# Performance work log

Measured on AMD Instinct MI355X. Metric: run time of the kernel, lower is better.

The kernel has to match this reference:

```python
import jax, jax.numpy as jnp
import numpy as np

RNN = 64      # rnn_hidden_dim
HID = 64      # hidden_dim
ENC = 3       # encoder_dim
NAG = 8       # n_agents
NACT = 14     # n_actions
CLIP = 0.2    # args.exp_clip (variance floor)
BN_EPS = 1e-5


def _bn(x, g, b):
    # BatchNorm1d in training mode: batch stats, biased variance
    m = x.mean(0)
    v = jnp.mean((x - m) ** 2, 0)
    return g * (x - m) * jax.lax.rsqrt(v + BN_EPS) + b


def setup_inputs() -> dict:
    key = jax.random.key(0)
    ks = jax.random.split(key, 16)
    B, INP = 8192, 96

    def w(k, shape, fan):
        return (jax.random.normal(k, shape, jnp.float32) / np.float32(np.sqrt(fan)))

    d = {}
    d["inputs"] = jax.random.normal(ks[0], (B * NAG, INP), jnp.float32)
    d["hidden_state"] = jax.random.normal(ks[1], (B * NAG, RNN), jnp.float32)
    d["noise"] = jax.random.normal(ks[2], (B, NAG, NAG * ENC), jnp.float32)
    d["fc1_w"] = w(ks[3], (INP, RNN), INP); d["fc1_b"] = jnp.zeros((RNN,), jnp.float32)
    d["w_ih"] = w(ks[4], (RNN, 3 * RNN), RNN); d["w_hh"] = w(ks[5], (RNN, 3 * RNN), RNN)
    d["b_ih"] = jnp.zeros((3 * RNN,), jnp.float32); d["b_hh"] = jnp.zeros((3 * RNN,), jnp.float32)
    d["aw1_w"] = w(ks[6], (RNN, HID), RNN); d["aw1_b"] = jnp.zeros((HID,), jnp.float32)
    d["aw_g"] = jnp.ones((HID,), jnp.float32); d["aw_be"] = jnp.zeros((HID,), jnp.float32)
    d["aw2_w"] = w(ks[7], (HID, 2 * NAG * ENC), HID); d["aw2_b"] = jnp.zeros((2 * NAG * ENC,), jnp.float32)
    d["po1_w"] = w(ks[8], (2 * RNN, HID), 2 * RNN); d["po1_b"] = jnp.zeros((HID,), jnp.float32)
    d["po_g"] = jnp.ones((HID,), jnp.float32); d["po_be"] = jnp.zeros((HID,), jnp.float32)
    d["po2_w"] = w(ks[9], (HID, 2 * ENC), HID); d["po2_b"] = jnp.zeros((2 * ENC,), jnp.float32)
    d["fc2_w"] = w(ks[10], (RNN + ENC * NAG, NACT), RNN + ENC * NAG); d["fc2_b"] = jnp.zeros((NACT,), jnp.float32)
    return d


def reference(inputs, hidden_state, noise,
              fc1_w, fc1_b, w_ih, w_hh, b_ih, b_hh,
              aw1_w, aw1_b, aw_g, aw_be, aw2_w, aw2_b,
              po1_w, po1_b, po_g, po_be, po2_w, po2_b,
              fc2_w, fc2_b):
    B, n, enc = noise.shape[0], NAG, ENC

    x = jax.nn.relu(inputs @ fc1_w + fc1_b)                      # [B*n, RNN]
    h_in = hidden_state.reshape(-1, RNN)

    # torch GRUCell
    gi = x @ w_ih + b_ih
    gh = h_in @ w_hh + b_hh
    ir, iz, i_n = jnp.split(gi, 3, axis=-1)
    hr, hz, h_n = jnp.split(gh, 3, axis=-1)
    r = jax.nn.sigmoid(ir + hr)
    z = jax.nn.sigmoid(iz + hz)
    nt = jnp.tanh(i_n + r * h_n)
    h = (1.0 - z) * nt + z * h_in                                # [B*n, RNN]

    # awareness encoder
    a = jax.nn.relu(_bn(h @ aw1_w + aw1_b, aw_g, aw_be))
    aw = (a @ aw2_w + aw2_b).reshape(B, n, 2 * n * enc)
    mu = aw[:, :, : n * enc]
    sigma = jnp.maximum(jnp.exp(aw[:, :, n * enc:]), CLIP)       # variance
    c = (mu + jnp.sqrt(sigma) * noise).reshape(-1, n * enc)      # rsample

    x_out = jnp.concatenate([h, c], axis=-1) @ fc2_w + fc2_b     # [B*n, NACT]

    # poster branch (training mode): all-pairs concat H[b, j, id] = [h[b,id], h[b,j]]
    hd = jax.lax.stop_gradient(h).reshape(B, n, RNN)
    Hi = jnp.broadcast_to(hd[:, None, :, :], (B, n, n, RNN))     # axis2 = id
    Hj = jnp.broadcast_to(hd[:, :, None, :], (B, n, n, RNN))     # axis1 = j
    H = jnp.concatenate([Hi, Hj], axis=-1).reshape(-1, 2 * RNN)  # [B*n*n, 2*RNN]

    p = jax.nn.relu(_bn(H @ po1_w + po1_b, po_g, po_be))
    out = (p @ po2_w + po2_b).reshape(B, n, 2 * n * enc)
    mu1 = out[:, :, : n * enc]
    sigma1 = jnp.maximum(jnp.exp(out[:, :, n * enc:]), CLIP)

    # KL between diagonal Gaussians (sigma, sigma1 are variances)
    kl = 0.5 * (jnp.log(sigma1 / sigma) + (sigma + (mu - mu1) ** 2) / sigma1 - 1.0)
    KL = kl.mean(axis=-1).mean(axis=-1, keepdims=True)           # [B, 1]
    return (x_out, h, KL)
```

## Files before the change

### kernel.cpp

```cpp
#include <hip/hip_runtime.h>
#include <math.h>

#define NROWS 65536
#define NB    8192
#define STAT_OFF  0
#define P2T_OFF   448
#define WPACK_OFF 832
#define OUT_XOUT 0
#define OUT_H    917504
#define OUT_KL   5111808

typedef __attribute__((ext_vector_type(8))) short bhalf8;
typedef __attribute__((ext_vector_type(4))) float floatx4;
typedef __attribute__((ext_vector_type(4))) unsigned short u16x4;

__device__ __forceinline__ float sigmf(float x) { return 1.0f / (1.0f + __expf(-x)); }
__device__ __forceinline__ float tanhfast(float x) {
    x = fminf(fmaxf(x, -15.f), 15.f);
    float e = __expf(-2.f * x);
    return (1.f - e) / (1.f + e);
}
__device__ __forceinline__ unsigned short f2bf(float f) {
    unsigned int u = __float_as_uint(f);
    u += 0x7FFFu + ((u >> 16) & 1u);
    return (unsigned short)(u >> 16);
}
__device__ __forceinline__ float bf2f(unsigned short s) {
    return __uint_as_float(((unsigned int)s) << 16);
}
__device__ __forceinline__ bhalf8 pack8(float4 a, float4 b) {
    bhalf8 r;
    r[0] = (short)f2bf(a.x); r[1] = (short)f2bf(a.y);
    r[2] = (short)f2bf(a.z); r[3] = (short)f2bf(a.w);
    r[4] = (short)f2bf(b.x); r[5] = (short)f2bf(b.y);
    r[6] = (short)f2bf(b.z); r[7] = (short)f2bf(b.w);
    return r;
}

__global__ void k_prep(const float* __restrict__ fc1_w,
                       const float* __restrict__ w_ih, const float* __restrict__ w_hh,
                       const float* __restrict__ aw1_w, const float* __restrict__ po1_w,
                       const float* __restrict__ aw2_w, const float* __restrict__ fc2_w,
                       const float* __restrict__ po2_w,
                       float* __restrict__ ws)
{
    const int t = threadIdx.x;
    if (blockIdx.x == 0) {
        for (int i = t; i < 448; i += 256) ws[STAT_OFF + i] = 0.f;
        for (int i = t; i < 384; i += 256) {
            int d = i >> 6, c = i & 63;
            ws[P2T_OFF + i] = po2_w[c * 6 + d];
        }
    }

    unsigned short* wpk = (unsigned short*)(ws + WPACK_OFF);
    for (int f = blockIdx.x * 256 + t; f < 5952; f += gridDim.x * 256) {
        int lane, c, tile;
        const float* src;
        int colbase, krowstride, kofs = 0, kmax = 1 << 30, colmax = 16;
        if (f < 768) {
            tile = f / 192; c = (f % 192) / 64; lane = f % 64;
            src = fc1_w; krowstride = 64; colbase = tile * 16;
        } else if (f < 3840) {
            int f2 = f - 768;
            tile = f2 / 128; c = (f2 % 128) / 64; lane = f2 % 64;
            if (tile < 12) { src = w_ih; colbase = tile * 16; }
            else           { src = w_hh; colbase = (tile - 12) * 16; }
            krowstride = 192;
        } else if (f < 5376) {
            int f3 = f - 3840;
            tile = f3 / 128; c = (f3 % 128) / 64; lane = f3 % 64;
            if (tile < 4)       { src = aw1_w; colbase = tile * 16; }
            else if (tile < 8)  { src = po1_w; colbase = (tile - 4) * 16; }
            else                { src = po1_w; colbase = (tile - 8) * 16; kofs = 64; }
            krowstride = 64;
        } else if (f < 5760) {
            int f4 = f - 5376;
            tile = f4 / 128; c = (f4 % 128) / 64; lane = f4 % 64;
            src = aw2_w; krowstride = 48; colbase = tile * 16;
        } else {
            int f5 = f - 5760;
            c = f5 / 64; lane = f5 % 64;
            src = fc2_w; krowstride = 14; colbase = 0;
            kmax = 88; colmax = 14;
        }
        int n = lane & 15, quad = lane >> 4;
        int col = colbase + n;
        unsigned short o[8];
        #pragma unroll
        for (int j = 0; j < 8; j++) {
            int k = c * 32 + quad * 8 + j + kofs;
            float v = (k < kmax && n < colmax) ? src[(size_t)k * krowstride + col] : 0.f;
            o[j] = f2bf(v);
        }
        u16x4 lo, hi;
        lo.x = o[0]; lo.y = o[1]; lo.z = o[2]; lo.w = o[3];
        hi.x = o[4]; hi.y = o[5]; hi.z = o[6]; hi.w = o[7];
        *(u16x4*)&wpk[f * 8]     = lo;
        *(u16x4*)&wpk[f * 8 + 4] = hi;
    }
}

__global__ __launch_bounds__(256, 4) void k_front(
    const float* __restrict__ inp, const float* __restrict__ hin,
    const float* __restrict__ fc1_b,
    const float* __restrict__ b_ih, const float* __restrict__ b_hh,
    const float* __restrict__ aw1_b,
    float* __restrict__ h_out, float* __restrict__ ws)
{
    __shared__ __align__(16) unsigned short s_xb[64 * 80];
    __shared__ float s_stat[448];

    const int t = threadIdx.x;
    const int row0 = blockIdx.x * 64;
    const int lane = t & 63;
    const int w = t >> 6;
    const int n16 = lane & 15;
    const int quad = lane >> 4;
    const int mrow = w * 16 + n16;

    for (int i = t; i < 448; i += 256) s_stat[i] = 0.f;
    __syncthreads();

    const bhalf8* wp1 = (const bhalf8*)((const unsigned short*)(ws + WPACK_OFF));
    const bhalf8* wp2 = wp1 + 768;
    const bhalf8* wp3 = wp1 + 3840;

    bhalf8 ai[3], ahf[2];
    {
        const float* gi = inp + (size_t)(row0 + mrow) * 96 + quad * 8;
        #pragma unroll
        for (int kc = 0; kc < 3; kc++)
            ai[kc] = pack8(*(const float4*)&gi[kc * 32], *(const float4*)&gi[kc * 32 + 4]);
        const float* gh = hin + (size_t)(row0 + mrow) * 64 + quad * 8;
        #pragma unroll
        for (int kc = 0; kc < 2; kc++)
            ahf[kc] = pack8(*(const float4*)&gh[kc * 32], *(const float4*)&gh[kc * 32 + 4]);
    }

    #pragma unroll
    for (int g = 0; g < 4; g++) {
        int col = g * 16 + n16;
        floatx4 d = {0.f, 0.f, 0.f, 0.f};
        d = __builtin_amdgcn_mfma_f32_16x16x32_bf16(ai[0], wp1[(g * 3 + 0) * 64 + lane], d, 0, 0, 0);
        d = __builtin_amdgcn_mfma_f32_16x16x32_bf16(ai[1], wp1[(g * 3 + 1) * 64 + lane], d, 0, 0, 0);
        d = __builtin_amdgcn_mfma_f32_16x16x32_bf16(ai[2], wp1[(g * 3 + 2) * 64 + lane], d, 0, 0, 0);
        float bb = fc1_b[col];
        #pragma unroll
        for (int q = 0; q < 4; q++)
            s_xb[(w * 16 + quad * 4 + q) * 80 + col] = f2bf(fmaxf(d[q] + bb, 0.f));
    }
    bhalf8 ax[2];
    ax[0] = *(const bhalf8*)&s_xb[mrow * 80 + 0  + quad * 8];
    ax[1] = *(const bhalf8*)&s_xb[mrow * 80 + 32 + quad * 8];

    #pragma unroll
    for (int g = 0; g < 4; g++) {
        int col = g * 16 + n16;
        floatx4 dr = {0.f, 0.f, 0.f, 0.f}, dz = {0.f, 0.f, 0.f, 0.f};
        floatx4 dn = {0.f, 0.f, 0.f, 0.f}, dh = {0.f, 0.f, 0.f, 0.f};
        dr = __builtin_amdgcn_mfma_f32_16x16x32_bf16(ax[0],  wp2[((0 + g) * 2 + 0) * 64 + lane], dr, 0, 0, 0);
        dr = __builtin_amdgcn_mfma_f32_16x16x32_bf16(ax[1],  wp2[((0 + g) * 2 + 1) * 64 + lane], dr, 0, 0, 0);
        dr = __builtin_amdgcn_mfma_f32_16x16x32_bf16(ahf[0], wp2[((12 + g) * 2 + 0) * 64 + lane], dr, 0, 0, 0);
        dr = __builtin_amdgcn_mfma_f32_16x16x32_bf16(ahf[1], wp2[((12 + g) * 2 + 1) * 64 + lane], dr, 0, 0, 0);
        dz = __builtin_amdgcn_mfma_f32_16x16x32_bf16(ax[0],  wp2[((4 + g) * 2 + 0) * 64 + lane], dz, 0, 0, 0);
        dz = __builtin_amdgcn_mfma_f32_16x16x32_bf16(ax[1],  wp2[((4 + g) * 2 + 1) * 64 + lane], dz, 0, 0, 0);
        dz = __builtin_amdgcn_mfma_f32_16x16x32_bf16(ahf[0], wp2[((16 + g) * 2 + 0) * 64 + lane], dz, 0, 0, 0);
        dz = __builtin_amdgcn_mfma_f32_16x16x32_bf16(ahf[1], wp2[((16 + g) * 2 + 1) * 64 + lane], dz, 0, 0, 0);
        dn = __builtin_amdgcn_mfma_f32_16x16x32_bf16(ax[0],  wp2[((8 + g) * 2 + 0) * 64 + lane], dn, 0, 0, 0);
        dn = __builtin_amdgcn_mfma_f32_16x16x32_bf16(ax[1],  wp2[((8 + g) * 2 + 1) * 64 + lane], dn, 0, 0, 0);
        dh = __builtin_amdgcn_mfma_f32_16x16x32_bf16(ahf[0], wp2[((20 + g) * 2 + 0) * 64 + lane], dh, 0, 0, 0);
        dh = __builtin_amdgcn_mfma_f32_16x16x32_bf16(ahf[1], wp2[((20 + g) * 2 + 1) * 64 + lane], dh, 0, 0, 0);
        float br_ = b_ih[col] + b_hh[col];
        float bz_ = b_ih[64 + col] + b_hh[64 + col];
        float bin_ = b_ih[128 + col];
        float bhn_ = b_hh[128 + col];
        #pragma unroll
        for (int q = 0; q < 4; q++) {
            int lrow = w * 16 + quad * 4 + q;
            size_t grow = (size_t)(row0 + lrow);
            float r  = sigmf(dr[q] + br_);
            float z  = sigmf(dz[q] + bz_);
            float nt = tanhfast(dn[q] + bin_ + r * (dh[q] + bhn_));
            float hp = hin[grow * 64 + col];
            float h  = (1.f - z) * nt + z * hp;
            h_out[grow * 64 + col] = h;
            s_xb[lrow * 80 + col] = f2bf(h);
        }
    }

    bhalf8 hh0 = *(const bhalf8*)&s_xb[mrow * 80 + 0  + quad * 8];
    bhalf8 hh1 = *(const bhalf8*)&s_xb[mrow * 80 + 32 + quad * 8];

    #pragma unroll
    for (int g = 0; g < 4; g++) {
        int col = g * 16 + n16;
        floatx4 da = {0.f, 0.f, 0.f, 0.f}, du = {0.f, 0.f, 0.f, 0.f}, dv = {0.f, 0.f, 0.f, 0.f};
        da = __builtin_amdgcn_mfma_f32_16x16x32_bf16(hh0, wp3[(g * 2 + 0) * 64 + lane], da, 0, 0, 0);
        da = __builtin_amdgcn_mfma_f32_16x16x32_bf16(hh1, wp3[(g * 2 + 1) * 64 + lane], da, 0, 0, 0);
        du = __builtin_amdgcn_mfma_f32_16x16x32_bf16(hh0, wp3[((4 + g) * 2 + 0) * 64 + lane], du, 0, 0, 0);
        du = __builtin_amdgcn_mfma_f32_16x16x32_bf16(hh1, wp3[((4 + g) * 2 + 1) * 64 + lane], du, 0, 0, 0);
        dv = __builtin_amdgcn_mfma_f32_16x16x32_bf16(hh0, wp3[((8 + g) * 2 + 0) * 64 + lane], dv, 0, 0, 0);
        dv = __builtin_amdgcn_mfma_f32_16x16x32_bf16(hh1, wp3[((8 + g) * 2 + 1) * 64 + lane], dv, 0, 0, 0);
        float ab = aw1_b[col];
        float s1 = 0.f, s2 = 0.f, su = 0.f, suq = 0.f, sv = 0.f, svq = 0.f;
        #pragma unroll
        for (int q = 0; q < 4; q++) {
            float a = da[q] + ab; s1 += a; s2 += a * a;
            float uv = du[q]; su += uv; suq += uv * uv;
            float vv = dv[q]; sv += vv; svq += vv * vv;
        }
        float u8 = su + __shfl_xor(su, 16, 64);
        float v8 = sv + __shfl_xor(sv, 16, 64);
        if ((quad & 1) == 0)
            atomicAdd(&s_stat[384 + col], u8 * v8 * (1.f / 64.f));
        float t1 = s1 + __shfl_xor(s1, 16, 64);   t1 += __shfl_xor(t1, 32, 64);
        float t2 = s2 + __shfl_xor(s2, 16, 64);   t2 += __shfl_xor(t2, 32, 64);
        float t3 = u8 + __shfl_xor(u8, 32, 64);
        float t4 = suq + __shfl_xor(suq, 16, 64); t4 += __shfl_xor(t4, 32, 64);
        float t5 = v8 + __shfl_xor(v8, 32, 64);
        float t6 = svq + __shfl_xor(svq, 16, 64); t6 += __shfl_xor(t6, 32, 64);
        if (quad == 0) {
            atomicAdd(&s_stat[col], t1);
            atomicAdd(&s_stat[64 + col], t2);
            atomicAdd(&s_stat[128 + col], t3);
            atomicAdd(&s_stat[192 + col], t4);
            atomicAdd(&s_stat[256 + col], t5);
            atomicAdd(&s_stat[320 + col], t6);
        }
    }
    __syncthreads();
    if (t < 64) {
        float* gs = ws + STAT_OFF;
        #pragma unroll
        for (int q = 0; q < 7; q++)
            atomicAdd(&gs[q * 64 + t], s_stat[q * 64 + t]);
    }
}

__global__ __launch_bounds__(256) void k_heads(
    const float* __restrict__ h_glob, const float* __restrict__ noise,
    const float* __restrict__ aw1_b, const float* __restrict__ aw2_b,
    const float* __restrict__ fc2_b, const float* __restrict__ po2_b,
    const float* __restrict__ aw_g, const float* __restrict__ aw_be,
    const float* __restrict__ po_g, const float* __restrict__ po_be,
    const float* __restrict__ po1_b,
    const float* __restrict__ ws, float* __restrict__ out)
{
    __shared__ __align__(16) unsigned short s_hb[32 * 104];
    __shared__ __align__(16) unsigned short s_Ub[32 * 80];
    __shared__ __align__(16) unsigned short s_Vb[32 * 80];
    __shared__ float s_ms[32 * 48];
    __shared__ __align__(16) float s_buf[32 * 48];
    __shared__ float s_dv[256];
    __shared__ float s_kl[32];

    const int t = threadIdx.x;
    const int row0 = blockIdx.x * 32;
    const int b0 = blockIdx.x * 4;
    const int lane = t & 63;
    const int w = t >> 6;
    const int n16 = lane & 15;
    const int quad = lane >> 4;
    const int mrow = w * 16 + n16;

    if (t < 64) {
        const float* st = ws + STAT_OFF;
        const float invN = 1.f / 65536.f;
        float am = st[t] * invN;
        float av = st[64 + t] * invN - am * am;
        float asc = aw_g[t] * rsqrtf(av + 1e-5f);
        s_dv[t] = asc;
        s_dv[64 + t] = aw_be[t] - asc * am;
        float Eu = st[128 + t] * invN;
        float vu = st[192 + t] * invN - Eu * Eu;
        float Ev = st[256 + t] * invN;
        float vv = st[320 + t] * invN - Ev * Ev;
        float cov = st[384 + t] * (1.f / 8192.f) - Eu * Ev;
        float my = Eu + Ev + po1_b[t];
        float vy = vu + vv + 2.f * cov;
        float psc = po_g[t] * rsqrtf(vy + 1e-5f);
        s_dv[128 + t] = psc;
        s_dv[192 + t] = po_be[t] + psc * (po1_b[t] - my);
    }

    {
        const float* gh = h_glob + (size_t)row0 * 64;
        for (int i = t; i < 512; i += 256) {
            int r = i >> 4, c4 = (i & 15) * 4;
            float4 v = *(const float4*)&gh[r * 64 + c4];
            u16x4 p; p.x = f2bf(v.x); p.y = f2bf(v.y); p.z = f2bf(v.z); p.w = f2bf(v.w);
            *(u16x4*)&s_hb[r * 104 + c4] = p;
        }
        if (t < 64) {
            int r = t >> 1, c4 = 88 + (t & 1) * 4;
            u16x4 z; z.x = 0; z.y = 0; z.z = 0; z.w = 0;
            *(u16x4*)&s_hb[r * 104 + c4] = z;
        }
    }
    __syncthreads();

    const bhalf8* wp3  = ((const bhalf8*)((const unsigned short*)(ws + WPACK_OFF))) + 3840;
    const bhalf8* wpa2 = wp3 + 1536;
    const bhalf8* wpf2 = wpa2 + 384;
    unsigned short* s_ab = (unsigned short*)s_buf;

    if (w < 2) {
        bhalf8 ah0 = *(const bhalf8*)&s_hb[mrow * 104 + 0  + quad * 8];
        bhalf8 ah1 = *(const bhalf8*)&s_hb[mrow * 104 + 32 + quad * 8];
        #pragma unroll
        for (int g = 0; g < 4; g++) {
            int col = g * 16 + n16;
            floatx4 da = {0.f, 0.f, 0.f, 0.f}, duu = {0.f, 0.f, 0.f, 0.f}, dvv = {0.f, 0.f, 0.f, 0.f};
            da  = __builtin_amdgcn_mfma_f32_16x16x32_bf16(ah0, wp3[(g * 2 + 0) * 64 + lane], da, 0, 0, 0);
            da  = __builtin_amdgcn_mfma_f32_16x16x32_bf16(ah1, wp3[(g * 2 + 1) * 64 + lane], da, 0, 0, 0);
            duu = __builtin_amdgcn_mfma_f32_16x16x32_bf16(ah0, wp3[((4 + g) * 2 + 0) * 64 + lane], duu, 0, 0, 0);
            duu = __builtin_amdgcn_mfma_f32_16x16x32_bf16(ah1, wp3[((4 + g) * 2 + 1) * 64 + lane], duu, 0, 0, 0);
            dvv = __builtin_amdgcn_mfma_f32_16x16x32_bf16(ah0, wp3[((8 + g) * 2 + 0) * 64 + lane], dvv, 0, 0, 0);
            dvv = __builtin_amdgcn_mfma_f32_16x16x32_bf16(ah1, wp3[((8 + g) * 2 + 1) * 64 + lane], dvv, 0, 0, 0);
            float ab = aw1_b[col];
            float asc = s_dv[col], ash = s_dv[64 + col];
            float psc = s_dv[128 + col], psh = s_dv[192 + col];
            #pragma unroll
            for (int q = 0; q < 4; q++) {
                int lrow = w * 16 + quad * 4 + q;
                s_ab[lrow * 80 + col] = f2bf(fmaxf(asc * (da[q] + ab) + ash, 0.f));
                s_Ub[lrow * 80 + col] = f2bf(psc * duu[q]);
                s_Vb[lrow * 80 + col] = f2bf(psc * dvv[q] + psh);
            }
        }
        bhalf8 aa0 = *(const bhalf8*)&s_ab[mrow * 80 + 0  + quad * 8];
        bhalf8 aa1 = *(const bhalf8*)&s_ab[mrow * 80 + 32 + quad * 8];
        #pragma unroll
        for (int g = 0; g < 3; g++) {
            floatx4 d = {0.f, 0.f, 0.f, 0.f};
            d = __builtin_amdgcn_mfma_f32_16x16x32_bf16(aa0, wpa2[(g * 2 + 0) * 64 + lane], d, 0, 0, 0);
            d = __builtin_amdgcn_mfma_f32_16x16x32_bf16(aa1, wpa2[(g * 2 + 1) * 64 + lane], d, 0, 0, 0);
            int col = g * 16 + n16;
            float bb = aw2_b[col];
            #pragma unroll
            for (int q = 0; q < 4; q++) {
                int lrow = w * 16 + quad * 4 + q;
                float v = d[q] + bb;
                s_ms[lrow * 48 + col] = (col < 24) ? v : fmaxf(__expf(v), 0.2f);
            }
        }
    }
    __syncthreads();

    for (int i = t; i < 768; i += 256) {
        int r = i / 24, m = i - r * 24;
        float c = s_ms[r * 48 + m] + sqrtf(s_ms[r * 48 + 24 + m]) * noise[(size_t)(row0 + r) * 24 + m];
        s_hb[r * 104 + 64 + m] = f2bf(c);
    }
    __syncthreads();

    if (w < 2) {
        bhalf8 hc0 = *(const bhalf8*)&s_hb[mrow * 104 + 0  + quad * 8];
        bhalf8 hc1 = *(const bhalf8*)&s_hb[mrow * 104 + 32 + quad * 8];
        bhalf8 hc2 = *(const bhalf8*)&s_hb[mrow * 104 + 64 + quad * 8];
        floatx4 d = {0.f, 0.f, 0.f, 0.f};
        d = __builtin_amdgcn_mfma_f32_16x16x32_bf16(hc0, wpf2[0 * 64 + lane], d, 0, 0, 0);
        d = __builtin_amdgcn_mfma_f32_16x16x32_bf16(hc1, wpf2[1 * 64 + lane], d, 0, 0, 0);
        d = __builtin_amdgcn_mfma_f32_16x16x32_bf16(hc2, wpf2[2 * 64 + lane], d, 0, 0, 0);
        if (n16 < 14) {
            float bb = fc2_b[n16];
            float* xout = out + OUT_XOUT;
            #pragma unroll
            for (int q = 0; q < 4; q++) {
                size_t grow = (size_t)(row0 + w * 16 + quad * 4 + q);
                xout[grow * 14 + n16] = d[q] + bb;
            }
        }
    }
    __syncthreads();

    float* s_out = s_buf;
    {
        const float* p2t = ws + P2T_OFF;
        const int bl = t >> 6;
        const int rem = t & 63;
        const int i_ = rem >> 3;
        const int j_ = rem & 7;
        float acc[6] = {0.f, 0.f, 0.f, 0.f, 0.f, 0.f};
        #pragma unroll
        for (int c = 0; c < 64; c += 8) {
            bhalf8 vb = *(const bhalf8*)&s_Vb[(bl * 8 + i_) * 80 + c];
            bhalf8 ub = *(const bhalf8*)&s_Ub[(bl * 8 + j_) * 80 + c];
            float p[8];
            #pragma unroll
            for (int q = 0; q < 8; q++)
                p[q] = fmaxf(bf2f((unsigned short)ub[q]) + bf2f((unsigned short)vb[q]), 0.f);
            #pragma unroll
            for (int d = 0; d < 6; d++) {
                const float* wd = &p2t[d * 64 + c];
                float s = 0.f;
                #pragma unroll
                for (int q = 0; q < 8; q++) s += p[q] * wd[q];
                acc[d] += s;
            }
        }
        #pragma unroll
        for (int d = 0; d < 6; d++)
            s_out[(bl * 8 + i_) * 48 + j_ * 6 + d] = acc[d] + po2_b[d];
    }
    __syncthreads();

    if (t < 32) {
        float s = 0.f;
        #pragma unroll 4
        for (int m = 0; m < 24; m++) {
            float mu0 = s_ms[t * 48 + m];
            float sg0 = s_ms[t * 48 + 24 + m];
            float mu1 = s_out[t * 48 + m];
            float sg1 = fmaxf(__expf(s_out[t * 48 + 24 + m]), 0.2f);
            float d0 = mu0 - mu1;
            s += __logf(sg1 / sg0) + (sg0 + d0 * d0) / sg1 - 1.f;
        }
        s_kl[t] = s;
    }
    __syncthreads();
    if (t < 4) {
        float s = 0.f;
        #pragma unroll
        for (int i = 0; i < 8; i++) s += s_kl[t * 8 + i];
        out[OUT_KL + b0 + t] = s * (0.5f / 192.f);
    }
}

extern "C" void kernel_launch(void* const* d_in, const int* in_sizes, int n_in,
                              void* d_out, int out_size, void* d_ws, size_t ws_size,
                              hipStream_t stream)
{
    (void)in_sizes; (void)n_in; (void)out_size; (void)ws_size;
    const float* inp   = (const float*)d_in[0];
    const float* hin   = (const float*)d_in[1];
    const float* noise = (const float*)d_in[2];
    const float* fc1_w = (const float*)d_in[3];
    const float* fc1_b = (const float*)d_in[4];
    const float* w_ih  = (const float*)d_in[5];
    const float* w_hh  = (const float*)d_in[6];
    const float* b_ih  = (const float*)d_in[7];
    const float* b_hh  = (const float*)d_in[8];
    const float* aw1_w = (const float*)d_in[9];
    const float* aw1_b = (const float*)d_in[10];
    const float* aw_g  = (const float*)d_in[11];
    const float* aw_be = (const float*)d_in[12];
    const float* aw2_w = (const float*)d_in[13];
    const float* aw2_b = (const float*)d_in[14];
    const float* po1_w = (const float*)d_in[15];
    const float* po1_b = (const float*)d_in[16];
    const float* po_g  = (const float*)d_in[17];
    const float* po_be = (const float*)d_in[18];
    const float* po2_w = (const float*)d_in[19];
    const float* po2_b = (const float*)d_in[20];
    const float* fc2_w = (const float*)d_in[21];
    const float* fc2_b = (const float*)d_in[22];
    float* out = (float*)d_out;
    float* ws  = (float*)d_ws;

    hipLaunchKernelGGL(k_prep,  dim3(24),   dim3(256), 0, stream,
                       fc1_w, w_ih, w_hh, aw1_w, po1_w, aw2_w, fc2_w, po2_w, ws);
    hipLaunchKernelGGL(k_front, dim3(1024), dim3(256), 0, stream,
                       inp, hin, fc1_b, b_ih, b_hh, aw1_b, out + OUT_H, ws);
    hipLaunchKernelGGL(k_heads, dim3(2048), dim3(256), 0, stream,
                       out + OUT_H, noise, aw1_b, aw2_b, fc2_b, po2_b,
                       aw_g, aw_be, po_g, po_be, po1_b, ws, out);
}
```

Measured before the change: 198.6 us.

## Register-block k_front over four row tiles per wave and split k_heads aw1 work

k_front now has each wave process 64 rows (four 16-row tiles), loading each packed weight fragment once and reusing it across four MFMA tiles. Blocks shrink to 128 threads handling 128 rows, with half the grid. k_heads spreads the aw1/poster projection MFMAs across all four waves instead of two. k_prep grid is doubled. This cuts repeated global weight-fragment loads but raises register pressure and lowers occupancy (launch bounds 128,1; only 512 blocks), and the k_prep grid change is unexplained.

```diff
diff --git a/kernel.cpp b/kernel.cpp
--- a/kernel.cpp
+++ b/kernel.cpp
@@ -101,124 +101,181 @@
     }
 }
 
-__global__ __launch_bounds__(256, 4) void k_front(
+__global__ __launch_bounds__(128, 1) void k_front(
     const float* __restrict__ inp, const float* __restrict__ hin,
     const float* __restrict__ fc1_b,
     const float* __restrict__ b_ih, const float* __restrict__ b_hh,
     const float* __restrict__ aw1_b,
     float* __restrict__ h_out, float* __restrict__ ws)
 {
-    __shared__ __align__(16) unsigned short s_xb[64 * 80];
+    __shared__ __align__(16) unsigned short s_xb[128 * 80];
     __shared__ float s_stat[448];
 
     const int t = threadIdx.x;
-    const int row0 = blockIdx.x * 64;
+    const int row0 = blockIdx.x * 128;
     const int lane = t & 63;
     const int w = t >> 6;
     const int n16 = lane & 15;
     const int quad = lane >> 4;
-    const int mrow = w * 16 + n16;
-
-    for (int i = t; i < 448; i += 256) s_stat[i] = 0.f;
+
+    for (int i = t; i < 448; i += 128) s_stat[i] = 0.f;
     __syncthreads();
 
     const bhalf8* wp1 = (const bhalf8*)((const unsigned short*)(ws + WPACK_OFF));
     const bhalf8* wp2 = wp1 + 768;
     const bhalf8* wp3 = wp1 + 3840;
 
-    bhalf8 ai[3], ahf[2];
-    {
-        const float* gi = inp + (size_t)(row0 + mrow) * 96 + quad * 8;
+    bhalf8 ai[4][3], ahf[4][2];
+    #pragma unroll
+    for (int u = 0; u < 4; u++) {
+        const int mr = w * 64 + u * 16 + n16;
+        const float* gi = inp + (size_t)(row0 + mr) * 96 + quad * 8;
         #pragma unroll
         for (int kc = 0; kc < 3; kc++)
-            ai[kc] = pack8(*(const float4*)&gi[kc * 32], *(const float4*)&gi[kc * 32 + 4]);
-        const float* gh = hin + (size_t)(row0 + mrow) * 64 + quad * 8;
+            ai[u][kc] = pack8(*(const float4*)&gi[kc * 32], *(const float4*)&gi[kc * 32 + 4]);
+        const float* gh = hin + (size_t)(row0 + mr) * 64 + quad * 8;
         #pragma unroll
         for (int kc = 0; kc < 2; kc++)
-            ahf[kc] = pack8(*(const float4*)&gh[kc * 32], *(const float4*)&gh[kc * 32 + 4]);
+            ahf[u][kc] = pack8(*(const float4*)&gh[kc * 32], *(const float4*)&gh[kc * 32 + 4]);
+    }
+
+    #pragma unroll
+    for (int g = 0; g < 4; g++) {
+        bhalf8 f0 = wp1[(g * 3 + 0) * 64 + lane];
+        bhalf8 f1 = wp1[(g * 3 + 1) * 64 + lane];
+        bhalf8 f2 = wp1[(g * 3 + 2) * 64 + lane];
+        int col = g * 16 + n16;
+        float bb = fc1_b[col];
+        #pragma unroll
+        for (int u = 0; u < 4; u++) {
+            floatx4 d = {0.f, 0.f, 0.f, 0.f};
+            d = __builtin_amdgcn_mfma_f32_16x16x32_bf16(ai[u][0], f0, d, 0, 0, 0);
+            d = __builtin_amdgcn_mfma_f32_16x16x32_bf16(ai[u][1], f1, d, 0, 0, 0);
+            d = __builtin_amdgcn_mfma_f32_16x16x32_bf16(ai[u][2], f2, d, 0, 0, 0);
+            #pragma unroll
+            for (int q = 0; q < 4; q++)
+                s_xb[(w * 64 + u * 16 + quad * 4 + q) * 80 + col] = f2bf(fmaxf(d[q] + bb, 0.f));
+        }
+    }
+    bhalf8 ax[4][2];
+    #pragma unroll
+    for (int u = 0; u < 4; u++) {
+        int mr = w * 64 + u * 16 + n16;
+        ax[u][0] = *(const bhalf8*)&s_xb[mr * 80 + 0  + quad * 8];
+        ax[u][1] = *(const bhalf8*)&s_xb[mr * 80 + 32 + quad * 8];
     }
 
     #pragma unroll
     for (int g = 0; g < 4; g++) {
         int col = g * 16 + n16;
-        floatx4 d = {0.f, 0.f, 0.f, 0.f};
-        d = __builtin_amdgcn_mfma_f32_16x16x32_bf16(ai[0], wp1[(g * 3 + 0) * 64 + lane], d, 0, 0, 0);
-        d = __builtin_amdgcn_mfma_f32_16x16x32_bf16(ai[1], wp1[(g * 3 + 1) * 64 + lane], d, 0, 0, 0);
-        d = __builtin_amdgcn_mfma_f32_16x16x32_bf16(ai[2], wp1[(g * 3 + 2) * 64 + lane], d, 0, 0, 0);
-        float bb = fc1_b[col];
-        #pragma unroll
-        for (int q = 0; q < 4; q++)
-            s_xb[(w * 16 + quad * 4 + q) * 80 + col] = f2bf(fmaxf(d[q] + bb, 0.f));
-    }
-    bhalf8 ax[2];
-    ax[0] = *(const bhalf8*)&s_xb[mrow * 80 + 0  + quad * 8];
-    ax[1] = *(const bhalf8*)&s_xb[mrow * 80 + 32 + quad * 8];
-
-    #pragma unroll
-    for (int g = 0; g < 4; g++) {
-        int col = g * 16 + n16;
-        floatx4 dr = {0.f, 0.f, 0.f, 0.f}, dz = {0.f, 0.f, 0.f, 0.f};
-        floatx4 dn = {0.f, 0.f, 0.f, 0.f}, dh = {0.f, 0.f, 0.f, 0.f};
-        dr = __builtin_amdgcn_mfma_f32_16x16x32_bf16(ax[0],  wp2[((0 + g) * 2 + 0) * 64 + lane], dr, 0, 0, 0);
-        dr = __builtin_amdgcn_mfma_f32_16x16x32_bf16(ax[1],  wp2[((0 + g) * 2 + 1) * 64 + lane], dr, 0, 0, 0);
-        dr = __builtin_amdgcn_mfma_f32_16x16x32_bf16(ahf[0], wp2[((12 + g) * 2 + 0) * 64 + lane], dr, 0, 0, 0);
-        dr = __builtin_amdgcn_mfma_f32_16x16x32_bf16(ahf[1], wp2[((12 + g) * 2 + 1) * 64 + lane], dr, 0, 0, 0);
-        dz = __builtin_amdgcn_mfma_f32_16x16x32_bf16(ax[0],  wp2[((4 + g) * 2 + 0) * 64 + lane], dz, 0, 0, 0);
-        dz = __builtin_amdgcn_mfma_f32_16x16x32_bf16(ax[1],  wp2[((4 + g) * 2 + 1) * 64 + lane], dz, 0, 0, 0);
-        dz = __builtin_amdgcn_mfma_f32_16x16x32_bf16(ahf[0], wp2[((16 + g) * 2 + 0) * 64 + lane], dz, 0, 0, 0);
-        dz = __builtin_amdgcn_mfma_f32_16x16x32_bf16(ahf[1], wp2[((16 + g) * 2 + 1) * 64 + lane], dz, 0, 0, 0);
-        dn = __builtin_amdgcn_mfma_f32_16x16x32_bf16(ax[0],  wp2[((8 + g) * 2 + 0) * 64 + lane], dn, 0, 0, 0);
-        dn = __builtin_amdgcn_mfma_f32_16x16x32_bf16(ax[1],  wp2[((8 + g) * 2 + 1) * 64 + lane], dn, 0, 0, 0);
-        dh = __builtin_amdgcn_mfma_f32_16x16x32_bf16(ahf[0], wp2[((20 + g) * 2 + 0) * 64 + lane], dh, 0, 0, 0);
-        dh = __builtin_amdgcn_mfma_f32_16x16x32_bf16(ahf[1], wp2[((20 + g) * 2 + 1) * 64 + lane], dh, 0, 0, 0);
+        bhalf8 fr0 = wp2[((0 + g) * 2 + 0) * 64 + lane];
+        bhalf8 fr1 = wp2[((0 + g) * 2 + 1) * 64 + lane];
+        bhalf8 fr2 = wp2[((12 + g) * 2 + 0) * 64 + lane];
+        bhalf8 fr3 = wp2[((12 + g) * 2 + 1) * 64 + lane];
+        bhalf8 fz0 = wp2[((4 + g) * 2 + 0) * 64 + lane];
+        bhalf8 fz1 = wp2[((4 + g) * 2 + 1) * 64 + lane];
+        bhalf8 fz2 = wp2[((16 + g) * 2 + 0) * 64 + lane];
+        bhalf8 fz3 = wp2[((16 + g) * 2 + 1) * 64 + lane];
+        bhalf8 fn0 = wp2[((8 + g) * 2 + 0) * 64 + lane];
+        bhalf8 fn1 = wp2[((8 + g) * 2 + 1) * 64 + lane];
+        bhalf8 fh0 = wp2[((20 + g) * 2 + 0) * 64 + lane];
+        bhalf8 fh1 = wp2[((20 + g) * 2 + 1) * 64 + lane];
+        floatx4 dr[4], dz[4], dn[4], dh[4];
+        #pragma unroll
+        for (int u = 0; u < 4; u++) {
+            floatx4 d = {0.f, 0.f, 0.f, 0.f};
+            d = __builtin_amdgcn_mfma_f32_16x16x32_bf16(ax[u][0], fr0, d, 0, 0, 0);
+            d = __builtin_amdgcn_mfma_f32_16x16x32_bf16(ax[u][1], fr1, d, 0, 0, 0);
+            d = __builtin_amdgcn_mfma_f32_16x16x32_bf16(ahf[u][0], fr2, d, 0, 0, 0);
+            d = __builtin_amdgcn_mfma_f32_16x16x32_bf16(ahf[u][1], fr3, d, 0, 0, 0);
+            dr[u] = d;
+            floatx4 e = {0.f, 0.f, 0.f, 0.f};
+            e = __builtin_amdgcn_mfma_f32_16x16x32_bf16(ax[u][0], fz0, e, 0, 0, 0);
+            e = __builtin_amdgcn_mfma_f32_16x16x32_bf16(ax[u][1], fz1, e, 0, 0, 0);
+            e = __builtin_amdgcn_mfma_f32_16x16x32_bf16(ahf[u][0], fz2, e, 0, 0, 0);
+            e = __builtin_amdgcn_mfma_f32_16x16x32_bf16(ahf[u][1], fz3, e, 0, 0, 0);
+            dz[u] = e;
+            floatx4 p = {0.f, 0.f, 0.f, 0.f};
+            p = __builtin_amdgcn_mfma_f32_16x16x32_bf16(ax[u][0], fn0, p, 0, 0, 0);
+            p = __builtin_amdgcn_mfma_f32_16x16x32_bf16(ax[u][1], fn1, p, 0, 0, 0);
+            dn[u] = p;
+            floatx4 s = {0.f, 0.f, 0.f, 0.f};
+            s = __builtin_amdgcn_mfma_f32_16x16x32_bf16(ahf[u][0], fh0, s, 0, 0, 0);
+            s = __builtin_amdgcn_mfma_f32_16x16x32_bf16(ahf[u][1], fh1, s, 0, 0, 0);
+            dh[u] = s;
+        }
         float br_ = b_ih[col] + b_hh[col];
         float bz_ = b_ih[64 + col] + b_hh[64 + col];
         float bin_ = b_ih[128 + col];
         float bhn_ = b_hh[128 + col];
         #pragma unroll
-        for (int q = 0; q < 4; q++) {
-            int lrow = w * 16 + quad * 4 + q;
-            size_t grow = (size_t)(row0 + lrow);
-            float r  = sigmf(dr[q] + br_);
-            float z  = sigmf(dz[q] + bz_);
-            float nt = tanhfast(dn[q] + bin_ + r * (dh[q] + bhn_));
-            float hp = hin[grow * 64 + col];
-            float h  = (1.f - z) * nt + z * hp;
-            h_out[grow * 64 + col] = h;
-            s_xb[lrow * 80 + col] = f2bf(h);
-        }
-    }
-
-    bhalf8 hh0 = *(const bhalf8*)&s_xb[mrow * 80 + 0  + quad * 8];
-    bhalf8 hh1 = *(const bhalf8*)&s_xb[mrow * 80 + 32 + quad * 8];
+        for (int u = 0; u < 4; u++) {
+            #pragma unroll
+            for (int q = 0; q < 4; q++) {
+                int lrow = w * 64 + u * 16 + quad * 4 + q;
+                size_t grow = (size_t)(row0 + lrow);
+                float r  = sigmf(dr[u][q] + br_);
+                float z  = sigmf(dz[u][q] + bz_);
+                float nt = tanhfast(dn[u][q] + bin_ + r * (dh[u][q] + bhn_));
+                float hp = hin[grow * 64 + col];
+                float h  = (1.f - z) * nt + z * hp;
+                h_out[grow * 64 + col] = h;
+                s_xb[lrow * 80 + col] = f2bf(h);
+            }
+        }
+    }
+
+    bhalf8 hh[4][2];
+    #pragma unroll
+    for (int u = 0; u < 4; u++) {
+        int mr = w * 64 + u * 16 + n16;
+        hh[u][0] = *(const bhalf8*)&s_xb[mr * 80 + 0  + quad * 8];
+        hh[u][1] = *(const bhalf8*)&s_xb[mr * 80 + 32 + quad * 8];
+    }
 
     #pragma unroll
     for (int g = 0; g < 4; g++) {
         int col = g * 16 + n16;
-        floatx4 da = {0.f, 0.f, 0.f, 0.f}, du = {0.f, 0.f, 0.f, 0.f}, dv = {0.f, 0.f, 0.f, 0.f};
-        da = __builtin_amdgcn_mfma_f32_16x16x32_bf16(hh0, wp3[(g * 2 + 0) * 64 + lane], da, 0, 0, 0);
-        da = __builtin_amdgcn_mfma_f32_16x16x32_bf16(hh1, wp3[(g * 2 + 1) * 64 + lane], da, 0, 0, 0);
-        du = __builtin_amdgcn_mfma_f32_16x16x32_bf16(hh0, wp3[((4 + g) * 2 + 0) * 64 + lane], du, 0, 0, 0);
-        du = __builtin_amdgcn_mfma_f32_16x16x32_bf16(hh1, wp3[((4 + g) * 2 + 1) * 64 + lane], du, 0, 0, 0);
-        dv = __builtin_amdgcn_mfma_f32_16x16x32_bf16(hh0, wp3[((8 + g) * 2 + 0) * 64 + lane], dv, 0, 0, 0);
-        dv = __builtin_amdgcn_mfma_f32_16x16x32_bf16(hh1, wp3[((8 + g) * 2 + 1) * 64 + lane], dv, 0, 0, 0);
+        bhalf8 fa0 = wp3[(g * 2 + 0) * 64 + lane];
+        bhalf8 fa1 = wp3[(g * 2 + 1) * 64 + lane];
+        bhalf8 fu0 = wp3[((4 + g) * 2 + 0) * 64 + lane];
+        bhalf8 fu1 = wp3[((4 + g) * 2 + 1) * 64 + lane];
+        bhalf8 fv0 = wp3[((8 + g) * 2 + 0) * 64 + lane];
+        bhalf8 fv1 = wp3[((8 + g) * 2 + 1) * 64 + lane];
         float ab = aw1_b[col];
-        float s1 = 0.f, s2 = 0.f, su = 0.f, suq = 0.f, sv = 0.f, svq = 0.f;
-        #pragma unroll
-        for (int q = 0; q < 4; q++) {
-            float a = da[q] + ab; s1 += a; s2 += a * a;
-            float uv = du[q]; su += uv; suq += uv * uv;
-            float vv = dv[q]; sv += vv; svq += vv * vv;
-        }
-        float u8 = su + __shfl_xor(su, 16, 64);
-        float v8 = sv + __shfl_xor(sv, 16, 64);
-        if ((quad & 1) == 0)
-            atomicAdd(&s_stat[384 + col], u8 * v8 * (1.f / 64.f));
+        float s1 = 0.f, s2 = 0.f, suq = 0.f, svq = 0.f;
+        float su[4], sv[4];
+        #pragma unroll
+        for (int u = 0; u < 4; u++) {
+            floatx4 da = {0.f, 0.f, 0.f, 0.f}, du = {0.f, 0.f, 0.f, 0.f}, dv = {0.f, 0.f, 0.f, 0.f};
+            da = __builtin_amdgcn_mfma_f32_16x16x32_bf16(hh[u][0], fa0, da, 0, 0, 0);
+            da = __builtin_amdgcn_mfma_f32_16x16x32_bf16(hh[u][1], fa1, da, 0, 0, 0);
+            du = __builtin_amdgcn_mfma_f32_16x16x32_bf16(hh[u][0], fu0, du, 0, 0, 0);
+            du = __builtin_amdgcn_mfma_f32_16x16x32_bf16(hh[u][1], fu1, du, 0, 0, 0);
+            dv = __builtin_amdgcn_mfma_f32_16x16x32_bf16(hh[u][0], fv0, dv, 0, 0, 0);
+            dv = __builtin_amdgcn_mfma_f32_16x16x32_bf16(hh[u][1], fv1, dv, 0, 0, 0);
+            su[u] = 0.f; sv[u] = 0.f;
+            #pragma unroll
+            for (int q = 0; q < 4; q++) {
+                float a = da[q] + ab; s1 += a; s2 += a * a;
+                float uv = du[q]; su[u] += uv; suq += uv * uv;
+                float vv = dv[q]; sv[u] += vv; svq += vv * vv;
+            }
+        }
+        float sut = 0.f, svt = 0.f;
+        #pragma unroll
+        for (int u = 0; u < 4; u++) {
+            float u8 = su[u] + __shfl_xor(su[u], 16, 64);
+            float v8 = sv[u] + __shfl_xor(sv[u], 16, 64);
+            if ((quad & 1) == 0)
+                atomicAdd(&s_stat[384 + col], u8 * v8 * (1.f / 64.f));
+            sut += su[u]; svt += sv[u];
+        }
         float t1 = s1 + __shfl_xor(s1, 16, 64);   t1 += __shfl_xor(t1, 32, 64);
         float t2 = s2 + __shfl_xor(s2, 16, 64);   t2 += __shfl_xor(t2, 32, 64);
-        float t3 = u8 + __shfl_xor(u8, 32, 64);
+        float t3 = sut + __shfl_xor(sut, 16, 64); t3 += __shfl_xor(t3, 32, 64);
         float t4 = suq + __shfl_xor(suq, 16, 64); t4 += __shfl_xor(t4, 32, 64);
-        float t5 = v8 + __shfl_xor(v8, 32, 64);
+        float t5 = svt + __shfl_xor(svt, 16, 64); t5 += __shfl_xor(t5, 32, 64);
         float t6 = svq + __shfl_xor(svq, 16, 64); t6 += __shfl_xor(t6, 32, 64);
         if (quad == 0) {
             atomicAdd(&s_stat[col], t1);
@@ -262,7 +319,9 @@
     const int w = t >> 6;
     const int n16 = lane & 15;
     const int quad = lane >> 4;
-    const int mrow = w * 16 + n16;
+    const int rh = w & 1;
+    const int grp = w >> 1;
+    const int arow = rh * 16 + n16;
 
     if (t < 64) {
         const float* st = ws + STAT_OFF;
@@ -305,32 +364,62 @@
     const bhalf8* wpf2 = wpa2 + 384;
     unsigned short* s_ab = (unsigned short*)s_buf;
 
+    {
+        bhalf8 ah0 = *(const bhalf8*)&s_hb[arow * 104 + 0  + quad * 8];
+        bhalf8 ah1 = *(const bhalf8*)&s_hb[arow * 104 + 32 + quad * 8];
+        if (grp == 0) {
+            #pragma unroll
+            for (int g = 0; g < 4; g++) {
+                int col = g * 16 + n16;
+                floatx4 da = {0.f, 0.f, 0.f, 0.f};
+                da = __builtin_amdgcn_mfma_f32_16x16x32_bf16(ah0, wp3[(g * 2 + 0) * 64 + lane], da, 0, 0, 0);
+                da = __builtin_amdgcn_mfma_f32_16x16x32_bf16(ah1, wp3[(g * 2 + 1) * 64 + lane], da, 0, 0, 0);
+                float ab = aw1_b[col];
+                float asc = s_dv[col], ash = s_dv[64 + col];
+                #pragma unroll
+                for (int q = 0; q < 4; q++)
+                    s_ab[(rh * 16 + quad * 4 + q) * 80 + col] = f2bf(fmaxf(asc * (da[q] + ab) + ash, 0.f));
+            }
+            #pragma unroll
+            for (int g = 0; g < 2; g++) {
+                int col = g * 16 + n16;
+                floatx4 du = {0.f, 0.f, 0.f, 0.f};
+                du = __builtin_amdgcn_mfma_f32_16x16x32_bf16(ah0, wp3[((4 + g) * 2 + 0) * 64 + lane], du, 0, 0, 0);
+                du = __builtin_amdgcn_mfma_f32_16x16x32_bf16(ah1, wp3[((4 + g) * 2 + 1) * 64 + lane], du, 0, 0, 0);
+                float psc = s_dv[128 + col];
+                #pragma unroll
+                for (int q = 0; q < 4; q++)
+                    s_Ub[(rh * 16 + quad * 4 + q) * 80 + col] = f2bf(psc * du[q]);
+            }
+        } else {
+            #pragma unroll
+            for (int g = 0; g < 4; g++) {
+                int col = g * 16 + n16;
+                floatx4 dv = {0.f, 0.f, 0.f, 0.f};
+                dv = __builtin_amdgcn_mfma_f32_16x16x32_bf16(ah0, wp3[((8 + g) * 2 + 0) * 64 + lane], dv, 0, 0, 0);
+                dv = __builtin_amdgcn_mfma_f32_16x16x32_bf16(ah1, wp3[((8 + g) * 2 + 1) * 64 + lane], dv, 0, 0, 0);
+                float psc = s_dv[128 + col], psh = s_dv[192 + col];
+                #pragma unroll
+                for (int q = 0; q < 4; q++)
+                    s_Vb[(rh * 16 + quad * 4 + q) * 80 + col] = f2bf(psc * dv[q] + psh);
+            }
+            #pragma unroll
+            for (int g = 2; g < 4; g++) {
+                int col = g * 16 + n16;
+                floatx4 du = {0.f, 0.f, 0.f, 0.f};
+                du = __builtin_amdgcn_mfma_f32_16x16x32_bf16(ah0, wp3[((4 + g) * 2 + 0) * 64 + lane], du, 0, 0, 0);
+                du = __builtin_amdgcn_mfma_f32_16x16x32_bf16(ah1, wp3[((4 + g) * 2 + 1) * 64 + lane], du, 0, 0, 0);
+                float psc = s_dv[128 + col];
+                #pragma unroll
+                for (int q = 0; q < 4; q++)
+                    s_Ub[(rh * 16 + quad * 4 + q) * 80 + col] = f2bf(psc * du[q]);
+            }
+        }
+    }
+
     if (w < 2) {
-        bhalf8 ah0 = *(const bhalf8*)&s_hb[mrow * 104 + 0  + quad * 8];
-        bhalf8 ah1 = *(const bhalf8*)&s_hb[mrow * 104 + 32 + quad * 8];
-        #pragma unroll
-        for (int g = 0; g < 4; g++) {
-            int col = g * 16 + n16;
-            floatx4 da = {0.f, 0.f, 0.f, 0.f}, duu = {0.f, 0.f, 0.f, 0.f}, dvv = {0.f, 0.f, 0.f, 0.f};
-            da  = __builtin_amdgcn_mfma_f32_16x16x32_bf16(ah0, wp3[(g * 2 + 0) * 64 + lane], da, 0, 0, 0);
-            da  = __builtin_amdgcn_mfma_f32_16x16x32_bf16(ah1, wp3[(g * 2 + 1) * 64 + lane], da, 0, 0, 0);
-            duu = __builtin_amdgcn_mfma_f32_16x16x32_bf16(ah0, wp3[((4 + g) * 2 + 0) * 64 + lane], duu, 0, 0, 0);
-            duu = __builtin_amdgcn_mfma_f32_16x16x32_bf16(ah1, wp3[((4 + g) * 2 + 1) * 64 + lane], duu, 0, 0, 0);
-            dvv = __builtin_amdgcn_mfma_f32_16x16x32_bf16(ah0, wp3[((8 + g) * 2 + 0) * 64 + lane], dvv, 0, 0, 0);
-            dvv = __builtin_amdgcn_mfma_f32_16x16x32_bf16(ah1, wp3[((8 + g) * 2 + 1) * 64 + lane], dvv, 0, 0, 0);
-            float ab = aw1_b[col];
-            float asc = s_dv[col], ash = s_dv[64 + col];
-            float psc = s_dv[128 + col], psh = s_dv[192 + col];
-            #pragma unroll
-            for (int q = 0; q < 4; q++) {
-                int lrow = w * 16 + quad * 4 + q;
-                s_ab[lrow * 80 + col] = f2bf(fmaxf(asc * (da[q] + ab) + ash, 0.f));
-                s_Ub[lrow * 80 + col] = f2bf(psc * duu[q]);
-                s_Vb[lrow * 80 + col] = f2bf(psc * dvv[q] + psh);
-            }
-        }
-        bhalf8 aa0 = *(const bhalf8*)&s_ab[mrow * 80 + 0  + quad * 8];
-        bhalf8 aa1 = *(const bhalf8*)&s_ab[mrow * 80 + 32 + quad * 8];
+        bhalf8 aa0 = *(const bhalf8*)&s_ab[arow * 80 + 0  + quad * 8];
+        bhalf8 aa1 = *(const bhalf8*)&s_ab[arow * 80 + 32 + quad * 8];
         #pragma unroll
         for (int g = 0; g < 3; g++) {
             floatx4 d = {0.f, 0.f, 0.f, 0.f};
@@ -356,9 +445,9 @@
     __syncthreads();
 
     if (w < 2) {
-        bhalf8 hc0 = *(const bhalf8*)&s_hb[mrow * 104 + 0  + quad * 8];
-        bhalf8 hc1 = *(const bhalf8*)&s_hb[mrow * 104 + 32 + quad * 8];
-        bhalf8 hc2 = *(const bhalf8*)&s_hb[mrow * 104 + 64 + quad * 8];
+        bhalf8 hc0 = *(const bhalf8*)&s_hb[arow * 104 + 0  + quad * 8];
+        bhalf8 hc1 = *(const bhalf8*)&s_hb[arow * 104 + 32 + quad * 8];
+        bhalf8 hc2 = *(const bhalf8*)&s_hb[arow * 104 + 64 + quad * 8];
         floatx4 d = {0.f, 0.f, 0.f, 0.f};
         d = __builtin_amdgcn_mfma_f32_16x16x32_bf16(hc0, wpf2[0 * 64 + lane], d, 0, 0, 0);
         d = __builtin_amdgcn_mfma_f32_16x16x32_bf16(hc1, wpf2[1 * 64 + lane], d, 0, 0, 0);
@@ -459,9 +548,9 @@
     float* out = (float*)d_out;
     float* ws  = (float*)d_ws;
 
-    hipLaunchKernelGGL(k_prep,  dim3(24),   dim3(256), 0, stream,
+    hipLaunchKernelGGL(k_prep,  dim3(48),   dim3(256), 0, stream,
                        fc1_w, w_ih, w_hh, aw1_w, po1_w, aw2_w, fc2_w, po2_w, ws);
-    hipLaunchKernelGGL(k_front, dim3(1024), dim3(256), 0, stream,
+    hipLaunchKernelGGL(k_front, dim3(512),  dim3(128), 0, stream,
                        inp, hin, fc1_b, b_ih, b_hh, aw1_b, out + OUT_H, ws);
     hipLaunchKernelGGL(k_heads, dim3(2048), dim3(256), 0, stream,
                        out + OUT_H, noise, aw1_b, aw2_b, fc2_b, po2_b,
```

Result: no change. 199.9 us (+0.7%).
